# Kernel optimization log

Hardware: AMD Instinct MI355X
Metric: run time of the kernel (lower is better)

The kernel has to match this reference:

```python
import jax, jax.numpy as jnp
import numpy as np

V = 100000   # vocab_size
H = 128      # hidden_dim
B = 4096     # number of sentences in the batch
T = 409600


def setup_inputs() -> dict:
    key = jax.random.key(0)
    k_tok, k_seg, k_y, k_e, k_wh, k_bh, k_wo, k_bo = jax.random.split(key, 8)
    token_ids = jax.random.randint(k_tok, (T,), 0, V, dtype=jnp.int32)
    segment_ids = jnp.sort(jax.random.randint(k_seg, (T,), 0, B, dtype=jnp.int32))
    y_true = jax.random.uniform(k_y, (B,), dtype=jnp.float32)
    # learned parameters (nn.Embedding ~ N(0,1); Linear ~ U(-1/sqrt(fan_in), +))
    embed_table = jax.random.normal(k_e, (V, H), dtype=jnp.float32)
    lim = 1.0 / np.sqrt(H)
    W_hid = jax.random.uniform(k_wh, (H, H), minval=-lim, maxval=lim, dtype=jnp.float32)
    b_hid = jax.random.uniform(k_bh, (H,), minval=-lim, maxval=lim, dtype=jnp.float32)
    W_out = jax.random.uniform(k_wo, (H, 1), minval=-lim, maxval=lim, dtype=jnp.float32)
    b_out = jax.random.uniform(k_bo, (1,), minval=-lim, maxval=lim, dtype=jnp.float32)
    return {
        "token_ids": token_ids,
        "segment_ids": segment_ids,
        "y_true": y_true,
        "embed_table": embed_table,
        "W_hid": W_hid,
        "b_hid": b_hid,
        "W_out": W_out,
        "b_out": b_out,
    }


def reference(token_ids, segment_ids, y_true, embed_table, W_hid, b_hid, W_out, b_out):
    # Fused gather + segment-mean (replaces the per-sentence Python loop).
    tok_emb = embed_table[token_ids]                                    # [T, H]
    sums = jax.ops.segment_sum(tok_emb, segment_ids, num_segments=B)   # [B, H]
    counts = jax.ops.segment_sum(jnp.ones((T,), tok_emb.dtype), segment_ids,
                                 num_segments=B)                        # [B]
    sent_embeds = sums / jnp.maximum(counts, 1.0)[:, None]             # [B, H]
    # Small MLP head: tanh hidden -> sigmoid scalar score.
    hid = jnp.tanh(sent_embeds @ W_hid + b_hid)                        # [B, H]
    probas = jax.nn.sigmoid(hid @ W_out + b_out).squeeze(-1)           # [B]
    # BCE with size_average=False (sum reduction); torch clamps log at -100.
    log_p = jnp.clip(jnp.log(probas), -100.0)
    log_1mp = jnp.clip(jnp.log1p(-probas), -100.0)
    total_loss = -jnp.sum(y_true * log_p + (1.0 - y_true) * log_1mp)
    return total_loss
```

## Files before the change

### kernel.cpp

```cpp
#include <hip/hip_runtime.h>
#include <math.h>

#define HDIM 128

__global__ void init_kernel(int* __restrict__ starts, int nB1, int Tval,
                            float* __restrict__ out) {
    int i = blockIdx.x * blockDim.x + threadIdx.x;
    if (i < nB1) starts[i] = Tval;
    if (i == 0) out[0] = 0.0f;
}

__global__ void seg_bounds_kernel(const int* __restrict__ seg,
                                  int* __restrict__ starts, int Tval) {
    int t = blockIdx.x * blockDim.x + threadIdx.x;
    if (t >= Tval) return;
    int b = seg[t];
    int a = (t == 0) ? -1 : seg[t - 1];
    for (int s = a + 1; s <= b; ++s) starts[s] = t;
}

__global__ __launch_bounds__(256) void gather_mean_kernel(
    const int* __restrict__ tok, const float* __restrict__ emb,
    const int* __restrict__ starts, float* __restrict__ sent, int Bval) {
    int wave = threadIdx.x >> 6;
    int lane = threadIdx.x & 63;
    int s = blockIdx.x * 4 + wave;
    if (s >= Bval) return;

    int t0 = starts[s];
    int t1 = starts[s + 1];
    int cnt = t1 - t0;

    int half = lane >> 5;
    int col  = lane & 31;

    float4 acc = make_float4(0.f, 0.f, 0.f, 0.f);

    int i = t0 + half;
    for (; i + 6 < t1; i += 8) {
        int ta = tok[i];
        int tb = tok[i + 2];
        int tc = tok[i + 4];
        int td = tok[i + 6];
        float4 fa = ((const float4*)(emb + (size_t)ta * HDIM))[col];
        float4 fb = ((const float4*)(emb + (size_t)tb * HDIM))[col];
        float4 fc = ((const float4*)(emb + (size_t)tc * HDIM))[col];
        float4 fd = ((const float4*)(emb + (size_t)td * HDIM))[col];
        acc.x += fa.x + fb.x + fc.x + fd.x;
        acc.y += fa.y + fb.y + fc.y + fd.y;
        acc.z += fa.z + fb.z + fc.z + fd.z;
        acc.w += fa.w + fb.w + fc.w + fd.w;
    }
    for (; i < t1; i += 2) {
        int ta = tok[i];
        float4 fa = ((const float4*)(emb + (size_t)ta * HDIM))[col];
        acc.x += fa.x; acc.y += fa.y; acc.z += fa.z; acc.w += fa.w;
    }

    acc.x += __shfl_down(acc.x, 32);
    acc.y += __shfl_down(acc.y, 32);
    acc.z += __shfl_down(acc.z, 32);
    acc.w += __shfl_down(acc.w, 32);

    if (half == 0) {
        float inv = 1.0f / (float)(cnt > 0 ? cnt : 1);
        acc.x *= inv; acc.y *= inv; acc.z *= inv; acc.w *= inv;
        ((float4*)(sent + (size_t)s * HDIM))[col] = acc;
    }
}

__global__ __launch_bounds__(256) void mlp_loss_kernel(
    const float* __restrict__ sent, const float* __restrict__ Wh,
    const float* __restrict__ bh, const float* __restrict__ Wo,
    const float* __restrict__ bo, const float* __restrict__ y,
    float* __restrict__ out, int Bval, int nblocks) {
    __shared__ float Wlds[HDIM * HDIM];
    __shared__ float slds[4][4 * HDIM];
    __shared__ float lred[4];

    for (int idx = threadIdx.x; idx < HDIM * HDIM / 4; idx += 256)
        ((float4*)Wlds)[idx] = ((const float4*)Wh)[idx];
    __syncthreads();

    int wave = threadIdx.x >> 6;
    int lane = threadIdx.x & 63;
    int j0 = lane * 2;

    float bh0 = bh[j0], bh1 = bh[j0 + 1];
    float wo0 = Wo[j0], wo1 = Wo[j0 + 1];
    float bov = bo[0];
    float lsum = 0.0f;

    const float2* W2 = (const float2*)Wlds;
    float* myld = &slds[wave][0];

    for (int base0 = blockIdx.x * 16; base0 < Bval; base0 += nblocks * 16) {
        int base = base0 + wave * 4;
        int rem = Bval - base;
        int nseg = rem < 4 ? (rem < 0 ? 0 : rem) : 4;

        for (int r = 0; r < nseg; ++r) {
            float2 v = ((const float2*)(sent + (size_t)(base + r) * HDIM))[lane];
            ((float2*)(myld + r * HDIM))[lane] = v;
        }

        float a00 = bh0, a01 = bh1, a10 = bh0, a11 = bh1;
        float a20 = bh0, a21 = bh1, a30 = bh0, a31 = bh1;
        for (int i = 0; i < HDIM; ++i) {
            float2 w = W2[i * (HDIM / 2) + lane];
            float s0 = myld[0 * HDIM + i];
            float s1 = myld[1 * HDIM + i];
            float s2 = myld[2 * HDIM + i];
            float s3 = myld[3 * HDIM + i];
            a00 = fmaf(s0, w.x, a00); a01 = fmaf(s0, w.y, a01);
            a10 = fmaf(s1, w.x, a10); a11 = fmaf(s1, w.y, a11);
            a20 = fmaf(s2, w.x, a20); a21 = fmaf(s2, w.y, a21);
            a30 = fmaf(s3, w.x, a30); a31 = fmaf(s3, w.y, a31);
        }

        float pr0 = tanhf(a00) * wo0 + tanhf(a01) * wo1;
        float pr1 = tanhf(a10) * wo0 + tanhf(a11) * wo1;
        float pr2 = tanhf(a20) * wo0 + tanhf(a21) * wo1;
        float pr3 = tanhf(a30) * wo0 + tanhf(a31) * wo1;
        for (int m = 1; m < 64; m <<= 1) {
            pr0 += __shfl_xor(pr0, m);
            pr1 += __shfl_xor(pr1, m);
            pr2 += __shfl_xor(pr2, m);
            pr3 += __shfl_xor(pr3, m);
        }

        if (lane == 0) {
            float prs[4] = {pr0, pr1, pr2, pr3};
            for (int r = 0; r < nseg; ++r) {
                float z = prs[r] + bov;
                float p = 1.0f / (1.0f + expf(-z));
                float lp  = fmaxf(logf(p),     -100.0f);
                float l1p = fmaxf(log1pf(-p),  -100.0f);
                float yv = y[base + r];
                lsum -= yv * lp + (1.0f - yv) * l1p;
            }
        }
    }

    if (lane == 0) lred[wave] = lsum;
    __syncthreads();
    if (threadIdx.x == 0) {
        float tot = lred[0] + lred[1] + lred[2] + lred[3];
        atomicAdd(out, tot);
    }
}

extern "C" void kernel_launch(void* const* d_in, const int* in_sizes, int n_in,
                              void* d_out, int out_size, void* d_ws, size_t ws_size,
                              hipStream_t stream) {
    const int*   tok = (const int*)d_in[0];
    const int*   seg = (const int*)d_in[1];
    const float* y   = (const float*)d_in[2];
    const float* emb = (const float*)d_in[3];
    const float* Wh  = (const float*)d_in[4];
    const float* bh  = (const float*)d_in[5];
    const float* Wo  = (const float*)d_in[6];
    const float* bo  = (const float*)d_in[7];

    int T_ = in_sizes[0];
    int B_ = in_sizes[2];

    float* out = (float*)d_out;

    int* starts = (int*)d_ws;
    size_t starts_bytes = ((size_t)(B_ + 1) * sizeof(int) + 255) & ~(size_t)255;
    float* sent = (float*)((char*)d_ws + starts_bytes);

    init_kernel<<<(B_ + 1 + 255) / 256, 256, 0, stream>>>(starts, B_ + 1, T_, out);
    seg_bounds_kernel<<<(T_ + 255) / 256, 256, 0, stream>>>(seg, starts, T_);
    gather_mean_kernel<<<(B_ + 3) / 4, 256, 0, stream>>>(tok, emb, starts, sent, B_);
    int nblocks = (B_ + 15) / 16;
    if (nblocks > 256) nblocks = 256;
    mlp_loss_kernel<<<nblocks, 256, 0, stream>>>(sent, Wh, bh, Wo, bo, y, out, B_, nblocks);
}
```

Before: 138.5 us.

## Fuse gather-mean with MLP loss head and fold init into segment bounds

Folds the init kernel into the segment-bounds kernel, which now fills trailing starts and zeroes the output. The gather-mean and MLP/loss kernels become one kernel: each wave computes one sentence mean into LDS, then does the 128x128 matvec reading W_hid from global/L2. The gather loop is unrolled to 8 outstanding loads per half-wave, with a masked tail. This drops two launches and the sentence-embedding round trip through global memory, at the cost of every wave re-reading W_hid and one atomic per block (1024 atomics instead of 256).

```diff
diff --git a/kernel.cpp b/kernel.cpp
--- a/kernel.cpp
+++ b/kernel.cpp
@@ -3,151 +3,126 @@
 
 #define HDIM 128
 
-__global__ void init_kernel(int* __restrict__ starts, int nB1, int Tval,
-                            float* __restrict__ out) {
-    int i = blockIdx.x * blockDim.x + threadIdx.x;
-    if (i < nB1) starts[i] = Tval;
-    if (i == 0) out[0] = 0.0f;
-}
-
 __global__ void seg_bounds_kernel(const int* __restrict__ seg,
-                                  int* __restrict__ starts, int Tval) {
+                                  int* __restrict__ starts, int Tval, int Bval,
+                                  float* __restrict__ out) {
     int t = blockIdx.x * blockDim.x + threadIdx.x;
     if (t >= Tval) return;
     int b = seg[t];
     int a = (t == 0) ? -1 : seg[t - 1];
     for (int s = a + 1; s <= b; ++s) starts[s] = t;
+    if (t == Tval - 1)
+        for (int s = b + 1; s <= Bval; ++s) starts[s] = Tval;
+    if (t == 0) out[0] = 0.0f;
 }
 
-__global__ __launch_bounds__(256) void gather_mean_kernel(
+__global__ __launch_bounds__(256) void fused_dan_kernel(
     const int* __restrict__ tok, const float* __restrict__ emb,
-    const int* __restrict__ starts, float* __restrict__ sent, int Bval) {
+    const int* __restrict__ starts, const float* __restrict__ Wh,
+    const float* __restrict__ bh, const float* __restrict__ Wo,
+    const float* __restrict__ bo, const float* __restrict__ y,
+    float* __restrict__ out, int Bval) {
+    __shared__ float slds[4][HDIM];
+    __shared__ float lred[4];
+
     int wave = threadIdx.x >> 6;
     int lane = threadIdx.x & 63;
     int s = blockIdx.x * 4 + wave;
-    if (s >= Bval) return;
-
-    int t0 = starts[s];
-    int t1 = starts[s + 1];
-    int cnt = t1 - t0;
-
-    int half = lane >> 5;
-    int col  = lane & 31;
-
-    float4 acc = make_float4(0.f, 0.f, 0.f, 0.f);
-
-    int i = t0 + half;
-    for (; i + 6 < t1; i += 8) {
-        int ta = tok[i];
-        int tb = tok[i + 2];
-        int tc = tok[i + 4];
-        int td = tok[i + 6];
-        float4 fa = ((const float4*)(emb + (size_t)ta * HDIM))[col];
-        float4 fb = ((const float4*)(emb + (size_t)tb * HDIM))[col];
-        float4 fc = ((const float4*)(emb + (size_t)tc * HDIM))[col];
-        float4 fd = ((const float4*)(emb + (size_t)td * HDIM))[col];
-        acc.x += fa.x + fb.x + fc.x + fd.x;
-        acc.y += fa.y + fb.y + fc.y + fd.y;
-        acc.z += fa.z + fb.z + fc.z + fd.z;
-        acc.w += fa.w + fb.w + fc.w + fd.w;
-    }
-    for (; i < t1; i += 2) {
-        int ta = tok[i];
-        float4 fa = ((const float4*)(emb + (size_t)ta * HDIM))[col];
-        acc.x += fa.x; acc.y += fa.y; acc.z += fa.z; acc.w += fa.w;
-    }
-
-    acc.x += __shfl_down(acc.x, 32);
-    acc.y += __shfl_down(acc.y, 32);
-    acc.z += __shfl_down(acc.z, 32);
-    acc.w += __shfl_down(acc.w, 32);
-
-    if (half == 0) {
-        float inv = 1.0f / (float)(cnt > 0 ? cnt : 1);
-        acc.x *= inv; acc.y *= inv; acc.z *= inv; acc.w *= inv;
-        ((float4*)(sent + (size_t)s * HDIM))[col] = acc;
-    }
-}
-
-__global__ __launch_bounds__(256) void mlp_loss_kernel(
-    const float* __restrict__ sent, const float* __restrict__ Wh,
-    const float* __restrict__ bh, const float* __restrict__ Wo,
-    const float* __restrict__ bo, const float* __restrict__ y,
-    float* __restrict__ out, int Bval, int nblocks) {
-    __shared__ float Wlds[HDIM * HDIM];
-    __shared__ float slds[4][4 * HDIM];
-    __shared__ float lred[4];
-
-    for (int idx = threadIdx.x; idx < HDIM * HDIM / 4; idx += 256)
-        ((float4*)Wlds)[idx] = ((const float4*)Wh)[idx];
-    __syncthreads();
-
-    int wave = threadIdx.x >> 6;
-    int lane = threadIdx.x & 63;
-    int j0 = lane * 2;
-
-    float bh0 = bh[j0], bh1 = bh[j0 + 1];
-    float wo0 = Wo[j0], wo1 = Wo[j0 + 1];
-    float bov = bo[0];
     float lsum = 0.0f;
 
-    const float2* W2 = (const float2*)Wlds;
-    float* myld = &slds[wave][0];
+    if (s < Bval) {
+        int t0 = starts[s];
+        int t1 = starts[s + 1];
+        int cnt = t1 - t0;
+        int half = lane >> 5;
+        int col  = lane & 31;
 
-    for (int base0 = blockIdx.x * 16; base0 < Bval; base0 += nblocks * 16) {
-        int base = base0 + wave * 4;
-        int rem = Bval - base;
-        int nseg = rem < 4 ? (rem < 0 ? 0 : rem) : 4;
+        float4 acc = make_float4(0.f, 0.f, 0.f, 0.f);
+        int i = t0 + half;
 
-        for (int r = 0; r < nseg; ++r) {
-            float2 v = ((const float2*)(sent + (size_t)(base + r) * HDIM))[lane];
-            ((float2*)(myld + r * HDIM))[lane] = v;
+        for (; i + 14 < t1; i += 16) {
+            int tix[8];
+            #pragma unroll
+            for (int k = 0; k < 8; ++k) tix[k] = tok[i + 2 * k];
+            float4 f[8];
+            #pragma unroll
+            for (int k = 0; k < 8; ++k)
+                f[k] = ((const float4*)(emb + (size_t)tix[k] * HDIM))[col];
+            #pragma unroll
+            for (int k = 0; k < 8; ++k) {
+                acc.x += f[k].x; acc.y += f[k].y;
+                acc.z += f[k].z; acc.w += f[k].w;
+            }
+        }
+        if (i < t1) {
+            int lim = t1 - 1;
+            int tix[8]; float msk[8];
+            #pragma unroll
+            for (int k = 0; k < 8; ++k) {
+                int ii = i + 2 * k;
+                tix[k] = tok[ii < lim ? ii : lim];
+                msk[k] = (ii < t1) ? 1.0f : 0.0f;
+            }
+            float4 f[8];
+            #pragma unroll
+            for (int k = 0; k < 8; ++k)
+                f[k] = ((const float4*)(emb + (size_t)tix[k] * HDIM))[col];
+            #pragma unroll
+            for (int k = 0; k < 8; ++k) {
+                acc.x = fmaf(f[k].x, msk[k], acc.x);
+                acc.y = fmaf(f[k].y, msk[k], acc.y);
+                acc.z = fmaf(f[k].z, msk[k], acc.z);
+                acc.w = fmaf(f[k].w, msk[k], acc.w);
+            }
         }
 
-        float a00 = bh0, a01 = bh1, a10 = bh0, a11 = bh1;
-        float a20 = bh0, a21 = bh1, a30 = bh0, a31 = bh1;
-        for (int i = 0; i < HDIM; ++i) {
-            float2 w = W2[i * (HDIM / 2) + lane];
-            float s0 = myld[0 * HDIM + i];
-            float s1 = myld[1 * HDIM + i];
-            float s2 = myld[2 * HDIM + i];
-            float s3 = myld[3 * HDIM + i];
-            a00 = fmaf(s0, w.x, a00); a01 = fmaf(s0, w.y, a01);
-            a10 = fmaf(s1, w.x, a10); a11 = fmaf(s1, w.y, a11);
-            a20 = fmaf(s2, w.x, a20); a21 = fmaf(s2, w.y, a21);
-            a30 = fmaf(s3, w.x, a30); a31 = fmaf(s3, w.y, a31);
+        acc.x += __shfl_down(acc.x, 32);
+        acc.y += __shfl_down(acc.y, 32);
+        acc.z += __shfl_down(acc.z, 32);
+        acc.w += __shfl_down(acc.w, 32);
+
+        if (half == 0) {
+            float inv = 1.0f / (float)(cnt > 0 ? cnt : 1);
+            acc.x *= inv; acc.y *= inv; acc.z *= inv; acc.w *= inv;
+            ((float4*)&slds[wave][0])[col] = acc;
         }
 
-        float pr0 = tanhf(a00) * wo0 + tanhf(a01) * wo1;
-        float pr1 = tanhf(a10) * wo0 + tanhf(a11) * wo1;
-        float pr2 = tanhf(a20) * wo0 + tanhf(a21) * wo1;
-        float pr3 = tanhf(a30) * wo0 + tanhf(a31) * wo1;
-        for (int m = 1; m < 64; m <<= 1) {
-            pr0 += __shfl_xor(pr0, m);
-            pr1 += __shfl_xor(pr1, m);
-            pr2 += __shfl_xor(pr2, m);
-            pr3 += __shfl_xor(pr3, m);
+        float2 bh2 = ((const float2*)bh)[lane];
+        float2 wo2 = ((const float2*)Wo)[lane];
+        float a0 = bh2.x, a1 = bh2.y;
+        const float2* W2 = (const float2*)Wh;
+        const float4* s4 = (const float4*)&slds[wave][0];
+        #pragma unroll 4
+        for (int q = 0; q < HDIM / 4; ++q) {
+            float4 sv = s4[q];
+            float2 w0 = W2[(4 * q + 0) * (HDIM / 2) + lane];
+            float2 w1 = W2[(4 * q + 1) * (HDIM / 2) + lane];
+            float2 w2 = W2[(4 * q + 2) * (HDIM / 2) + lane];
+            float2 w3 = W2[(4 * q + 3) * (HDIM / 2) + lane];
+            a0 = fmaf(sv.x, w0.x, a0); a1 = fmaf(sv.x, w0.y, a1);
+            a0 = fmaf(sv.y, w1.x, a0); a1 = fmaf(sv.y, w1.y, a1);
+            a0 = fmaf(sv.z, w2.x, a0); a1 = fmaf(sv.z, w2.y, a1);
+            a0 = fmaf(sv.w, w3.x, a0); a1 = fmaf(sv.w, w3.y, a1);
         }
 
+        float pr = tanhf(a0) * wo2.x + tanhf(a1) * wo2.y;
+        #pragma unroll
+        for (int mm = 1; mm < 64; mm <<= 1) pr += __shfl_xor(pr, mm);
+
         if (lane == 0) {
-            float prs[4] = {pr0, pr1, pr2, pr3};
-            for (int r = 0; r < nseg; ++r) {
-                float z = prs[r] + bov;
-                float p = 1.0f / (1.0f + expf(-z));
-                float lp  = fmaxf(logf(p),     -100.0f);
-                float l1p = fmaxf(log1pf(-p),  -100.0f);
-                float yv = y[base + r];
-                lsum -= yv * lp + (1.0f - yv) * l1p;
-            }
+            float z = pr + bo[0];
+            float p = 1.0f / (1.0f + expf(-z));
+            float lp  = fmaxf(logf(p),    -100.0f);
+            float l1p = fmaxf(log1pf(-p), -100.0f);
+            float yv = y[s];
+            lsum = -(yv * lp + (1.0f - yv) * l1p);
         }
     }
 
     if (lane == 0) lred[wave] = lsum;
     __syncthreads();
-    if (threadIdx.x == 0) {
-        float tot = lred[0] + lred[1] + lred[2] + lred[3];
-        atomicAdd(out, tot);
-    }
+    if (threadIdx.x == 0)
+        atomicAdd(out, lred[0] + lred[1] + lred[2] + lred[3]);
 }
 
 extern "C" void kernel_launch(void* const* d_in, const int* in_sizes, int n_in,
@@ -166,15 +141,9 @@
     int B_ = in_sizes[2];
 
     float* out = (float*)d_out;
+    int* starts = (int*)d_ws;
 
-    int* starts = (int*)d_ws;
-    size_t starts_bytes = ((size_t)(B_ + 1) * sizeof(int) + 255) & ~(size_t)255;
-    float* sent = (float*)((char*)d_ws + starts_bytes);
-
-    init_kernel<<<(B_ + 1 + 255) / 256, 256, 0, stream>>>(starts, B_ + 1, T_, out);
-    seg_bounds_kernel<<<(T_ + 255) / 256, 256, 0, stream>>>(seg, starts, T_);
-    gather_mean_kernel<<<(B_ + 3) / 4, 256, 0, stream>>>(tok, emb, starts, sent, B_);
-    int nblocks = (B_ + 15) / 16;
-    if (nblocks > 256) nblocks = 256;
-    mlp_loss_kernel<<<nblocks, 256, 0, stream>>>(sent, Wh, bh, Wo, bo, y, out, B_, nblocks);
+    seg_bounds_kernel<<<(T_ + 255) / 256, 256, 0, stream>>>(seg, starts, T_, B_, out);
+    fused_dan_kernel<<<(B_ + 3) / 4, 256, 0, stream>>>(tok, emb, starts, Wh, bh, Wo,
+                                                       bo, y, out, B_);
 }
```

Measured after the change: 133.8 us. 3.4% less time.
